# Performance work log

Measured on AMD Instinct MI355X. Metric: run time of the kernel, lower is better.

## Reference

```python
import jax, jax.numpy as jnp
import numpy as np


def _ternary(x, delta):
    # {-1, 0, +1} thresholded at +/- delta
    return jnp.where(x > delta, 1.0, jnp.where(x < -delta, -1.0, 0.0)).astype(x.dtype)


def setup_inputs() -> dict:
    key = jax.random.key(0)
    kx, kw = jax.random.split(key)
    x = jax.random.normal(kx, (8192, 4096), dtype=jnp.float32)
    weight = jax.random.normal(kw, (4096, 4096), dtype=jnp.float32) * 0.02
    return {"x": x, "weight": weight}


def reference(x, weight):
    # TernaryActivation: delta = 0.1 * mean|x|
    x_q = _ternary(x, 0.1 * jnp.mean(jnp.abs(x)))
    # TernaryQuantize: delta = 0.05 * mean|w|, scaled by alpha = mean|w|
    w_abs_mean = jnp.mean(jnp.abs(weight))
    w_q = w_abs_mean * _ternary(weight, 0.05 * w_abs_mean)
    # F.linear(x_q, w_q) = x_q @ w_q.T
    return jnp.einsum('bi,oi->bo', x_q, w_q)
```

## Files before the change

kernel.cpp:

```cpp
#include <hip/hip_runtime.h>
#include <stdint.h>

typedef __attribute__((ext_vector_type(4))) int i32x4;
typedef __attribute__((ext_vector_type(8))) int i32x8;
typedef __attribute__((ext_vector_type(4))) float f32x4;

#define MROWS 8192L
#define NCOLS 4096L
#define KDIM  4096L

#define XQ_BYTES   (MROWS * KDIM / 2)
#define WQ_BYTES   (NCOLS * KDIM / 2)
#define SCAL_OFF   (XQ_BYTES + WQ_BYTES)

__global__ __launch_bounds__(256) void k_reduce_abs(const float* __restrict__ x,
                                                    const float* __restrict__ w,
                                                    float* __restrict__ partials) {
    __shared__ float sm[256];
    int b = blockIdx.x;
    int t = threadIdx.x;
    const float4* v;
    long base;
    if (b < 512) { v = (const float4*)x; base = (long)b * 16384; }
    else         { v = (const float4*)w; base = (long)(b - 512) * 16384; }
    float s = 0.f;
    for (int i = t; i < 16384; i += 256) {
        float4 q = v[base + i];
        s += fabsf(q.x) + fabsf(q.y) + fabsf(q.z) + fabsf(q.w);
    }
    sm[t] = s;
    __syncthreads();
    for (int off = 128; off > 0; off >>= 1) {
        if (t < off) sm[t] += sm[t + off];
        __syncthreads();
    }
    if (t == 0) partials[b] = sm[0];
}

__global__ __launch_bounds__(256) void k_finalize(float* __restrict__ scal) {
    const float* partials = scal + 4;
    __shared__ double sm[256];
    int t = threadIdx.x;

    double sx = 0.0;
    for (int i = t; i < 512; i += 256) sx += (double)partials[i];
    sm[t] = sx;
    __syncthreads();
    for (int off = 128; off > 0; off >>= 1) {
        if (t < off) sm[t] += sm[t + off];
        __syncthreads();
    }
    double SX = sm[0];
    __syncthreads();

    double sw = (double)partials[512 + t];
    sm[t] = sw;
    __syncthreads();
    for (int off = 128; off > 0; off >>= 1) {
        if (t < off) sm[t] += sm[t + off];
        __syncthreads();
    }
    if (t == 0) {
        float meanx = (float)(SX / 33554432.0);
        float meanw = (float)(sm[0] / 16777216.0);
        scal[0] = 0.1f * meanx;
        scal[1] = 0.05f * meanw;
        scal[2] = meanw;
    }
}

__device__ __forceinline__ unsigned int nib4(float v, float delta) {
    return v > delta ? 2u : (v < -delta ? 10u : 0u);
}

__global__ __launch_bounds__(256) void k_quant4(const float* __restrict__ src,
                                                unsigned int* __restrict__ dst,
                                                const float* __restrict__ scal,
                                                int scal_idx, long total8) {
    float delta = scal[scal_idx];
    long i0 = (long)blockIdx.x * 256 + threadIdx.x;
    long stride = (long)gridDim.x * 256;
    const float4* s4 = (const float4*)src;
    for (long i = i0; i < total8; i += stride) {
        float4 q0 = s4[2 * i];
        float4 q1 = s4[2 * i + 1];
        unsigned int wd = nib4(q0.x, delta)
                        | (nib4(q0.y, delta) << 4)
                        | (nib4(q0.z, delta) << 8)
                        | (nib4(q0.w, delta) << 12)
                        | (nib4(q1.x, delta) << 16)
                        | (nib4(q1.y, delta) << 20)
                        | (nib4(q1.z, delta) << 24)
                        | (nib4(q1.w, delta) << 28);
        dst[i] = wd;
    }
}

#define GLOAD_LDS16(g, l)                                                             \
    __builtin_amdgcn_global_load_lds((const __attribute__((address_space(1))) void*)(g), \
                                     (__attribute__((address_space(3))) void*)(l),       \
                                     16, 0, 0)

#define MK8(v) __builtin_shufflevector((v), (v), 0, 1, 2, 3, -1, -1, -1, -1)

#define MFMA4(a, b, c)                                                        \
    __builtin_amdgcn_mfma_scale_f32_16x16x128_f8f6f4(MK8(a), MK8(b), (c),     \
        4, 4, 0, 0x7F7F7F7F, 0, 0x7F7F7F7F)

__global__ __launch_bounds__(512, 2) void k_gemm(const signed char* __restrict__ Xq,
                                                 const signed char* __restrict__ Wq,
                                                 float* __restrict__ out,
                                                 const float* __restrict__ scal) {
    __shared__ __attribute__((aligned(16))) signed char lds[131072];

    const float alpha = scal[2];

    int bid = (int)blockIdx.x;
    bid = (bid & 7) * 64 + (bid >> 3);
    int bm = bid >> 4;
    int bn = bid & 15;
    long row0 = (long)bm * 256;
    long col0 = (long)bn * 256;

    int t = threadIdx.x;
    int lane = t & 63;
    int wid = t >> 6;
    int wm = wid >> 2;
    int wn = wid & 3;

    int srow = t >> 2;
    int scol = ((t & 3) ^ ((t >> 3) & 3)) * 16;
    const signed char* Asrc = Xq + (row0 + srow) * 2048 + scol;
    const signed char* Bsrc = Wq + (col0 + srow) * 2048 + scol;
    const int ldst = wid * 1024;

#define STAGE(slot, g1) do {                                                   \
    const signed char* a_ = Asrc + (long)(g1) * 64;                            \
    const signed char* b_ = Bsrc + (long)(g1) * 64;                            \
    signed char* la_ = lds + (slot) * 32768 + ldst;                            \
    signed char* lb_ = la_ + 16384;                                            \
    GLOAD_LDS16(a_, la_);                                                      \
    GLOAD_LDS16(a_ + 128L * 2048, la_ + 8192);                                 \
    GLOAD_LDS16(b_, lb_);                                                      \
    GLOAD_LDS16(b_ + 128L * 2048, lb_ + 8192);                                 \
} while (0)

    int fr = lane & 15;
    int ck = (((lane >> 4) ^ ((fr >> 1) & 3)) << 4);
    int aoff = (wm * 128 + fr) * 64;
    int boff = 16384 + (wn * 64 + fr) * 64;

    f32x4 acc[8][4];
#pragma unroll
    for (int i = 0; i < 8; ++i)
#pragma unroll
        for (int j = 0; j < 4; ++j)
            acc[i][j] = (f32x4){0.f, 0.f, 0.f, 0.f};

    STAGE(0, 0);
    STAGE(1, 1);
    STAGE(2, 2);

    for (int g = 0; g < 32; ++g) {
        int slot = g & 3;
        __builtin_amdgcn_s_barrier();
        if (g < 29) {
            STAGE((g + 3) & 3, g + 3);
            asm volatile("s_waitcnt vmcnt(12)" ::: "memory");
        } else if (g == 29) {
            asm volatile("s_waitcnt vmcnt(8)" ::: "memory");
        } else if (g == 30) {
            asm volatile("s_waitcnt vmcnt(4)" ::: "memory");
        } else {
            asm volatile("s_waitcnt vmcnt(0)" ::: "memory");
        }
        __builtin_amdgcn_s_barrier();
        __builtin_amdgcn_sched_barrier(0);

        const signed char* A = lds + slot * 32768 + aoff;
        const signed char* B = lds + slot * 32768 + boff;

        i32x4 a0, a1, a2, a3, b0, b1, b2, b3;
        a0 = *(const i32x4*)(A + 0 * 1024 + ck);
        a1 = *(const i32x4*)(A + 1 * 1024 + ck);
        a2 = *(const i32x4*)(A + 2 * 1024 + ck);
        a3 = *(const i32x4*)(A + 3 * 1024 + ck);
        b0 = *(const i32x4*)(B + 0 * 1024 + ck);
        b1 = *(const i32x4*)(B + 1 * 1024 + ck);
        __builtin_amdgcn_s_setprio(1);
        acc[0][0] = MFMA4(a0, b0, acc[0][0]);
        acc[1][0] = MFMA4(a1, b0, acc[1][0]);
        acc[2][0] = MFMA4(a2, b0, acc[2][0]);
        acc[3][0] = MFMA4(a3, b0, acc[3][0]);
        acc[0][1] = MFMA4(a0, b1, acc[0][1]);
        acc[1][1] = MFMA4(a1, b1, acc[1][1]);
        acc[2][1] = MFMA4(a2, b1, acc[2][1]);
        acc[3][1] = MFMA4(a3, b1, acc[3][1]);
        __builtin_amdgcn_s_setprio(0);
        b2 = *(const i32x4*)(B + 2 * 1024 + ck);
        b3 = *(const i32x4*)(B + 3 * 1024 + ck);
        __builtin_amdgcn_s_setprio(1);
        acc[0][2] = MFMA4(a0, b2, acc[0][2]);
        acc[1][2] = MFMA4(a1, b2, acc[1][2]);
        acc[2][2] = MFMA4(a2, b2, acc[2][2]);
        acc[3][2] = MFMA4(a3, b2, acc[3][2]);
        acc[0][3] = MFMA4(a0, b3, acc[0][3]);
        acc[1][3] = MFMA4(a1, b3, acc[1][3]);
        acc[2][3] = MFMA4(a2, b3, acc[2][3]);
        acc[3][3] = MFMA4(a3, b3, acc[3][3]);
        __builtin_amdgcn_s_setprio(0);
        a0 = *(const i32x4*)(A + 4 * 1024 + ck);
        a1 = *(const i32x4*)(A + 5 * 1024 + ck);
        a2 = *(const i32x4*)(A + 6 * 1024 + ck);
        a3 = *(const i32x4*)(A + 7 * 1024 + ck);
        __builtin_amdgcn_s_setprio(1);
        acc[4][0] = MFMA4(a0, b0, acc[4][0]);
        acc[5][0] = MFMA4(a1, b0, acc[5][0]);
        acc[6][0] = MFMA4(a2, b0, acc[6][0]);
        acc[7][0] = MFMA4(a3, b0, acc[7][0]);
        acc[4][1] = MFMA4(a0, b1, acc[4][1]);
        acc[5][1] = MFMA4(a1, b1, acc[5][1]);
        acc[6][1] = MFMA4(a2, b1, acc[6][1]);
        acc[7][1] = MFMA4(a3, b1, acc[7][1]);
        __builtin_amdgcn_s_setprio(0);
        __builtin_amdgcn_s_setprio(1);
        acc[4][2] = MFMA4(a0, b2, acc[4][2]);
        acc[5][2] = MFMA4(a1, b2, acc[5][2]);
        acc[6][2] = MFMA4(a2, b2, acc[6][2]);
        acc[7][2] = MFMA4(a3, b2, acc[7][2]);
        acc[4][3] = MFMA4(a0, b3, acc[4][3]);
        acc[5][3] = MFMA4(a1, b3, acc[5][3]);
        acc[6][3] = MFMA4(a2, b3, acc[6][3]);
        acc[7][3] = MFMA4(a3, b3, acc[7][3]);
        __builtin_amdgcn_s_setprio(0);
    }

#pragma unroll
    for (int mi = 0; mi < 8; ++mi) {
#pragma unroll
        for (int ni = 0; ni < 4; ++ni) {
            long col = col0 + wn * 64 + ni * 16 + (lane & 15);
            long rowb = row0 + wm * 128 + mi * 16 + (lane >> 4) * 4;
#pragma unroll
            for (int r = 0; r < 4; ++r) {
                out[(rowb + r) * NCOLS + col] = alpha * acc[mi][ni][r];
            }
        }
    }
#undef STAGE
}

extern "C" void kernel_launch(void* const* d_in, const int* in_sizes, int n_in,
                              void* d_out, int out_size, void* d_ws, size_t ws_size,
                              hipStream_t stream) {
    const float* x = (const float*)d_in[0];
    const float* w = (const float*)d_in[1];
    float* out = (float*)d_out;

    uint8_t* ws = (uint8_t*)d_ws;
    signed char* Xq = (signed char*)ws;
    signed char* Wq = (signed char*)(ws + XQ_BYTES);
    float* scal = (float*)(ws + SCAL_OFF);

    k_reduce_abs<<<768, 256, 0, stream>>>(x, w, scal + 4);
    k_finalize<<<1, 256, 0, stream>>>(scal);
    k_quant4<<<2048, 256, 0, stream>>>(x, (unsigned int*)Xq, scal, 0, MROWS * KDIM / 8);
    k_quant4<<<1024, 256, 0, stream>>>(w, (unsigned int*)Wq, scal, 1, NCOLS * KDIM / 8);
    k_gemm<<<512, 512, 0, stream>>>(Xq, Wq, out, scal);
}
```

Before: 164.1 us.

## Interleave GEMM global-to-LDS prefetch with MFMA phases and merge quant kernels

The per-iteration bulk STAGE prefetch at loop top is split into four single global_load_lds issues, one inserted before each MFMA phase. Each phase is fenced with barriers and lgkmcnt waits, which shifts the vmcnt wait thresholds. This spreads memory issue across the compute phases so loads overlap with MFMA work. The two quantization launches are also merged into one kernel dispatched by block index. The extra barriers per phase add synchronization cost and could stall waves.

```diff
diff --git a/kernel.cpp b/kernel.cpp
--- a/kernel.cpp
+++ b/kernel.cpp
@@ -2,7 +2,6 @@
 #include <stdint.h>
 
 typedef __attribute__((ext_vector_type(4))) int i32x4;
-typedef __attribute__((ext_vector_type(8))) int i32x8;
 typedef __attribute__((ext_vector_type(4))) float f32x4;
 
 #define MROWS 8192L
@@ -73,13 +72,23 @@
     return v > delta ? 2u : (v < -delta ? 10u : 0u);
 }
 
-__global__ __launch_bounds__(256) void k_quant4(const float* __restrict__ src,
-                                                unsigned int* __restrict__ dst,
-                                                const float* __restrict__ scal,
-                                                int scal_idx, long total8) {
-    float delta = scal[scal_idx];
-    long i0 = (long)blockIdx.x * 256 + threadIdx.x;
-    long stride = (long)gridDim.x * 256;
+__global__ __launch_bounds__(256) void k_quant4(const float* __restrict__ x,
+                                                const float* __restrict__ w,
+                                                unsigned int* __restrict__ xq,
+                                                unsigned int* __restrict__ wq,
+                                                const float* __restrict__ scal) {
+    int b = blockIdx.x;
+    const float* src;
+    unsigned int* dst;
+    float delta;
+    long i0, stride, total8;
+    if (b < 2048) {
+        src = x; dst = xq; delta = scal[0];
+        i0 = (long)b * 256 + threadIdx.x; stride = 2048L * 256; total8 = MROWS * KDIM / 8;
+    } else {
+        src = w; dst = wq; delta = scal[1];
+        i0 = (long)(b - 2048) * 256 + threadIdx.x; stride = 1024L * 256; total8 = NCOLS * KDIM / 8;
+    }
     const float4* s4 = (const float4*)src;
     for (long i = i0; i < total8; i += stride) {
         float4 q0 = s4[2 * i];
@@ -107,6 +116,15 @@
     __builtin_amdgcn_mfma_scale_f32_16x16x128_f8f6f4(MK8(a), MK8(b), (c),     \
         4, 4, 0, 0x7F7F7F7F, 0, 0x7F7F7F7F)
 
+#define PHASE_PRE()  do {                                   \
+    __builtin_amdgcn_s_barrier();                           \
+    asm volatile("s_waitcnt lgkmcnt(0)" ::: "memory");      \
+    __builtin_amdgcn_sched_barrier(0);                      \
+    __builtin_amdgcn_s_setprio(1); } while (0)
+#define PHASE_POST() do {                                   \
+    __builtin_amdgcn_s_setprio(0);                          \
+    __builtin_amdgcn_s_barrier(); } while (0)
+
 __global__ __launch_bounds__(512, 2) void k_gemm(const signed char* __restrict__ Xq,
                                                  const signed char* __restrict__ Wq,
                                                  float* __restrict__ out,
@@ -163,11 +181,7 @@
 
     for (int g = 0; g < 32; ++g) {
         int slot = g & 3;
-        __builtin_amdgcn_s_barrier();
-        if (g < 29) {
-            STAGE((g + 3) & 3, g + 3);
-            asm volatile("s_waitcnt vmcnt(12)" ::: "memory");
-        } else if (g == 29) {
+        if (g <= 29) {
             asm volatile("s_waitcnt vmcnt(8)" ::: "memory");
         } else if (g == 30) {
             asm volatile("s_waitcnt vmcnt(4)" ::: "memory");
@@ -179,6 +193,11 @@
 
         const signed char* A = lds + slot * 32768 + aoff;
         const signed char* B = lds + slot * 32768 + boff;
+        bool st = (g <= 28);
+        const signed char* a3_ = Asrc + (long)(g + 3) * 64;
+        const signed char* b3_ = Bsrc + (long)(g + 3) * 64;
+        signed char* la3_ = lds + ((g + 3) & 3) * 32768 + ldst;
+        signed char* lb3_ = la3_ + 16384;
 
         i32x4 a0, a1, a2, a3, b0, b1, b2, b3;
         a0 = *(const i32x4*)(A + 0 * 1024 + ck);
@@ -187,7 +206,8 @@
         a3 = *(const i32x4*)(A + 3 * 1024 + ck);
         b0 = *(const i32x4*)(B + 0 * 1024 + ck);
         b1 = *(const i32x4*)(B + 1 * 1024 + ck);
-        __builtin_amdgcn_s_setprio(1);
+        if (st) GLOAD_LDS16(a3_, la3_);
+        PHASE_PRE();
         acc[0][0] = MFMA4(a0, b0, acc[0][0]);
         acc[1][0] = MFMA4(a1, b0, acc[1][0]);
         acc[2][0] = MFMA4(a2, b0, acc[2][0]);
@@ -196,10 +216,11 @@
         acc[1][1] = MFMA4(a1, b1, acc[1][1]);
         acc[2][1] = MFMA4(a2, b1, acc[2][1]);
         acc[3][1] = MFMA4(a3, b1, acc[3][1]);
-        __builtin_amdgcn_s_setprio(0);
+        PHASE_POST();
         b2 = *(const i32x4*)(B + 2 * 1024 + ck);
         b3 = *(const i32x4*)(B + 3 * 1024 + ck);
-        __builtin_amdgcn_s_setprio(1);
+        if (st) GLOAD_LDS16(a3_ + 128L * 2048, la3_ + 8192);
+        PHASE_PRE();
         acc[0][2] = MFMA4(a0, b2, acc[0][2]);
         acc[1][2] = MFMA4(a1, b2, acc[1][2]);
         acc[2][2] = MFMA4(a2, b2, acc[2][2]);
@@ -208,12 +229,13 @@
         acc[1][3] = MFMA4(a1, b3, acc[1][3]);
         acc[2][3] = MFMA4(a2, b3, acc[2][3]);
         acc[3][3] = MFMA4(a3, b3, acc[3][3]);
-        __builtin_amdgcn_s_setprio(0);
+        PHASE_POST();
         a0 = *(const i32x4*)(A + 4 * 1024 + ck);
         a1 = *(const i32x4*)(A + 5 * 1024 + ck);
         a2 = *(const i32x4*)(A + 6 * 1024 + ck);
         a3 = *(const i32x4*)(A + 7 * 1024 + ck);
-        __builtin_amdgcn_s_setprio(1);
+        if (st) GLOAD_LDS16(b3_, lb3_);
+        PHASE_PRE();
         acc[4][0] = MFMA4(a0, b0, acc[4][0]);
         acc[5][0] = MFMA4(a1, b0, acc[5][0]);
         acc[6][0] = MFMA4(a2, b0, acc[6][0]);
@@ -222,8 +244,9 @@
         acc[5][1] = MFMA4(a1, b1, acc[5][1]);
         acc[6][1] = MFMA4(a2, b1, acc[6][1]);
         acc[7][1] = MFMA4(a3, b1, acc[7][1]);
-        __builtin_amdgcn_s_setprio(0);
-        __builtin_amdgcn_s_setprio(1);
+        PHASE_POST();
+        if (st) GLOAD_LDS16(b3_ + 128L * 2048, lb3_ + 8192);
+        PHASE_PRE();
         acc[4][2] = MFMA4(a0, b2, acc[4][2]);
         acc[5][2] = MFMA4(a1, b2, acc[5][2]);
         acc[6][2] = MFMA4(a2, b2, acc[6][2]);
@@ -264,7 +287,6 @@
 
     k_reduce_abs<<<768, 256, 0, stream>>>(x, w, scal + 4);
     k_finalize<<<1, 256, 0, stream>>>(scal);
-    k_quant4<<<2048, 256, 0, stream>>>(x, (unsigned int*)Xq, scal, 0, MROWS * KDIM / 8);
-    k_quant4<<<1024, 256, 0, stream>>>(w, (unsigned int*)Wq, scal, 1, NCOLS * KDIM / 8);
+    k_quant4<<<3072, 256, 0, stream>>>(x, w, (unsigned int*)Xq, (unsigned int*)Wq, scal);
     k_gemm<<<512, 512, 0, stream>>>(Xq, Wq, out, scal);
 }
```

Measured after the change: 161.7 us. No clear change (-1.5%).

## Switch GEMM to 32x32x64 FP4 MFMA with matching LDS layout; merge quant launches

Applied to the files above, without the earlier changes.

Replaces the 16x16x128 scaled FP4 MFMA with the 32x32x64 variant. The global-to-LDS staging is re-laid out so each lane reads its 16-byte operand fragment contiguously, and the epilogue is adjusted to the 32x32 output layout. The intent is fewer MFMA and LDS-read instructions per tile and higher matrix throughput, at the cost of a new LDS layout that may introduce bank conflicts. The two quantization launches are also merged into one kernel to save a launch.

```diff
diff --git a/kernel.cpp b/kernel.cpp
--- a/kernel.cpp
+++ b/kernel.cpp
@@ -2,8 +2,7 @@
 #include <stdint.h>
 
 typedef __attribute__((ext_vector_type(4))) int i32x4;
-typedef __attribute__((ext_vector_type(8))) int i32x8;
-typedef __attribute__((ext_vector_type(4))) float f32x4;
+typedef __attribute__((ext_vector_type(16))) float f32x16;
 
 #define MROWS 8192L
 #define NCOLS 4096L
@@ -73,13 +72,23 @@
     return v > delta ? 2u : (v < -delta ? 10u : 0u);
 }
 
-__global__ __launch_bounds__(256) void k_quant4(const float* __restrict__ src,
-                                                unsigned int* __restrict__ dst,
-                                                const float* __restrict__ scal,
-                                                int scal_idx, long total8) {
-    float delta = scal[scal_idx];
-    long i0 = (long)blockIdx.x * 256 + threadIdx.x;
-    long stride = (long)gridDim.x * 256;
+__global__ __launch_bounds__(256) void k_quant4(const float* __restrict__ x,
+                                                const float* __restrict__ w,
+                                                unsigned int* __restrict__ xq,
+                                                unsigned int* __restrict__ wq,
+                                                const float* __restrict__ scal) {
+    int b = blockIdx.x;
+    const float* src;
+    unsigned int* dst;
+    float delta;
+    long i0, stride, total8;
+    if (b < 2048) {
+        src = x; dst = xq; delta = scal[0];
+        i0 = (long)b * 256 + threadIdx.x; stride = 2048L * 256; total8 = MROWS * KDIM / 8;
+    } else {
+        src = w; dst = wq; delta = scal[1];
+        i0 = (long)(b - 2048) * 256 + threadIdx.x; stride = 1024L * 256; total8 = NCOLS * KDIM / 8;
+    }
     const float4* s4 = (const float4*)src;
     for (long i = i0; i < total8; i += stride) {
         float4 q0 = s4[2 * i];
@@ -103,8 +112,8 @@
 
 #define MK8(v) __builtin_shufflevector((v), (v), 0, 1, 2, 3, -1, -1, -1, -1)
 
-#define MFMA4(a, b, c)                                                        \
-    __builtin_amdgcn_mfma_scale_f32_16x16x128_f8f6f4(MK8(a), MK8(b), (c),     \
+#define MFMA32(a, b, c)                                                       \
+    __builtin_amdgcn_mfma_scale_f32_32x32x64_f8f6f4(MK8(a), MK8(b), (c),      \
         4, 4, 0, 0x7F7F7F7F, 0, 0x7F7F7F7F)
 
 __global__ __launch_bounds__(512, 2) void k_gemm(const signed char* __restrict__ Xq,
@@ -128,34 +137,38 @@
     int wm = wid >> 2;
     int wn = wid & 3;
 
-    int srow = t >> 2;
-    int scol = ((t & 3) ^ ((t >> 3) & 3)) * 16;
-    const signed char* Asrc = Xq + (row0 + srow) * 2048 + scol;
-    const signed char* Bsrc = Wq + (col0 + srow) * 2048 + scol;
-    const int ldst = wid * 1024;
+    const signed char* sp[4];
+    int ldoff[4];
+#pragma unroll
+    for (int j = 0; j < 4; ++j) {
+        int g = wid * 4 + j;
+        ldoff[j] = g * 1024;
+        if (g < 16) {
+            long grow = row0 + (g >> 3) * 128 + ((g >> 1) & 3) * 32 + (lane & 31);
+            sp[j] = Xq + grow * 2048 + (g & 1) * 32 + (lane >> 5) * 16;
+        } else {
+            int h = g - 16;
+            long grow = col0 + (h >> 2) * 64 + ((h >> 1) & 1) * 32 + (lane & 31);
+            sp[j] = Wq + grow * 2048 + (h & 1) * 32 + (lane >> 5) * 16;
+        }
+    }
 
 #define STAGE(slot, g1) do {                                                   \
-    const signed char* a_ = Asrc + (long)(g1) * 64;                            \
-    const signed char* b_ = Bsrc + (long)(g1) * 64;                            \
-    signed char* la_ = lds + (slot) * 32768 + ldst;                            \
-    signed char* lb_ = la_ + 16384;                                            \
-    GLOAD_LDS16(a_, la_);                                                      \
-    GLOAD_LDS16(a_ + 128L * 2048, la_ + 8192);                                 \
-    GLOAD_LDS16(b_, lb_);                                                      \
-    GLOAD_LDS16(b_ + 128L * 2048, lb_ + 8192);                                 \
+    signed char* sb_ = lds + (slot) * 32768;                                   \
+    _Pragma("unroll")                                                          \
+    for (int j_ = 0; j_ < 4; ++j_)                                             \
+        GLOAD_LDS16(sp[j_] + (long)(g1) * 64, sb_ + ldoff[j_]);                \
 } while (0)
 
-    int fr = lane & 15;
-    int ck = (((lane >> 4) ^ ((fr >> 1) & 3)) << 4);
-    int aoff = (wm * 128 + fr) * 64;
-    int boff = 16384 + (wn * 64 + fr) * 64;
-
-    f32x4 acc[8][4];
-#pragma unroll
-    for (int i = 0; i < 8; ++i)
-#pragma unroll
-        for (int j = 0; j < 4; ++j)
-            acc[i][j] = (f32x4){0.f, 0.f, 0.f, 0.f};
+    const signed char* Ab = lds + wm * 8192 + lane * 16;
+    const signed char* Bb = lds + 16384 + wn * 4096 + lane * 16;
+
+    f32x16 acc[4][2];
+#pragma unroll
+    for (int i = 0; i < 4; ++i)
+#pragma unroll
+        for (int j = 0; j < 2; ++j)
+            acc[i][j] = (f32x16){0.f};
 
     STAGE(0, 0);
     STAGE(1, 1);
@@ -177,73 +190,55 @@
         __builtin_amdgcn_s_barrier();
         __builtin_amdgcn_sched_barrier(0);
 
-        const signed char* A = lds + slot * 32768 + aoff;
-        const signed char* B = lds + slot * 32768 + boff;
-
-        i32x4 a0, a1, a2, a3, b0, b1, b2, b3;
-        a0 = *(const i32x4*)(A + 0 * 1024 + ck);
-        a1 = *(const i32x4*)(A + 1 * 1024 + ck);
-        a2 = *(const i32x4*)(A + 2 * 1024 + ck);
-        a3 = *(const i32x4*)(A + 3 * 1024 + ck);
-        b0 = *(const i32x4*)(B + 0 * 1024 + ck);
-        b1 = *(const i32x4*)(B + 1 * 1024 + ck);
+        const signed char* A = Ab + slot * 32768;
+        const signed char* B = Bb + slot * 32768;
+
+        i32x4 a00, a01, a10, a11, a20, a21, a30, a31;
+        i32x4 b00, b01, b10, b11;
+        b00 = *(const i32x4*)(B + 0 * 1024);
+        b01 = *(const i32x4*)(B + 1 * 1024);
+        b10 = *(const i32x4*)(B + 2 * 1024);
+        b11 = *(const i32x4*)(B + 3 * 1024);
+        a00 = *(const i32x4*)(A + 0 * 1024);
+        a01 = *(const i32x4*)(A + 1 * 1024);
+        a10 = *(const i32x4*)(A + 2 * 1024);
+        a11 = *(const i32x4*)(A + 3 * 1024);
         __builtin_amdgcn_s_setprio(1);
-        acc[0][0] = MFMA4(a0, b0, acc[0][0]);
-        acc[1][0] = MFMA4(a1, b0, acc[1][0]);
-        acc[2][0] = MFMA4(a2, b0, acc[2][0]);
-        acc[3][0] = MFMA4(a3, b0, acc[3][0]);
-        acc[0][1] = MFMA4(a0, b1, acc[0][1]);
-        acc[1][1] = MFMA4(a1, b1, acc[1][1]);
-        acc[2][1] = MFMA4(a2, b1, acc[2][1]);
-        acc[3][1] = MFMA4(a3, b1, acc[3][1]);
+        acc[0][0] = MFMA32(a00, b00, acc[0][0]);
+        acc[0][1] = MFMA32(a00, b10, acc[0][1]);
+        acc[1][0] = MFMA32(a10, b00, acc[1][0]);
+        acc[1][1] = MFMA32(a10, b10, acc[1][1]);
+        acc[0][0] = MFMA32(a01, b01, acc[0][0]);
+        acc[0][1] = MFMA32(a01, b11, acc[0][1]);
+        acc[1][0] = MFMA32(a11, b01, acc[1][0]);
+        acc[1][1] = MFMA32(a11, b11, acc[1][1]);
         __builtin_amdgcn_s_setprio(0);
-        b2 = *(const i32x4*)(B + 2 * 1024 + ck);
-        b3 = *(const i32x4*)(B + 3 * 1024 + ck);
+        a20 = *(const i32x4*)(A + 4 * 1024);
+        a21 = *(const i32x4*)(A + 5 * 1024);
+        a30 = *(const i32x4*)(A + 6 * 1024);
+        a31 = *(const i32x4*)(A + 7 * 1024);
         __builtin_amdgcn_s_setprio(1);
-        acc[0][2] = MFMA4(a0, b2, acc[0][2]);
-        acc[1][2] = MFMA4(a1, b2, acc[1][2]);
-        acc[2][2] = MFMA4(a2, b2, acc[2][2]);
-        acc[3][2] = MFMA4(a3, b2, acc[3][2]);
-        acc[0][3] = MFMA4(a0, b3, acc[0][3]);
-        acc[1][3] = MFMA4(a1, b3, acc[1][3]);
-        acc[2][3] = MFMA4(a2, b3, acc[2][3]);
-        acc[3][3] = MFMA4(a3, b3, acc[3][3]);
+        acc[2][0] = MFMA32(a20, b00, acc[2][0]);
+        acc[2][1] = MFMA32(a20, b10, acc[2][1]);
+        acc[3][0] = MFMA32(a30, b00, acc[3][0]);
+        acc[3][1] = MFMA32(a30, b10, acc[3][1]);
+        acc[2][0] = MFMA32(a21, b01, acc[2][0]);
+        acc[2][1] = MFMA32(a21, b11, acc[2][1]);
+        acc[3][0] = MFMA32(a31, b01, acc[3][0]);
+        acc[3][1] = MFMA32(a31, b11, acc[3][1]);
         __builtin_amdgcn_s_setprio(0);
-        a0 = *(const i32x4*)(A + 4 * 1024 + ck);
-        a1 = *(const i32x4*)(A + 5 * 1024 + ck);
-        a2 = *(const i32x4*)(A + 6 * 1024 + ck);
-        a3 = *(const i32x4*)(A + 7 * 1024 + ck);
-        __builtin_amdgcn_s_setprio(1);
-        acc[4][0] = MFMA4(a0, b0, acc[4][0]);
-        acc[5][0] = MFMA4(a1, b0, acc[5][0]);
-        acc[6][0] = MFMA4(a2, b0, acc[6][0]);
-        acc[7][0] = MFMA4(a3, b0, acc[7][0]);
-        acc[4][1] = MFMA4(a0, b1, acc[4][1]);
-        acc[5][1] = MFMA4(a1, b1, acc[5][1]);
-        acc[6][1] = MFMA4(a2, b1, acc[6][1]);
-        acc[7][1] = MFMA4(a3, b1, acc[7][1]);
-        __builtin_amdgcn_s_setprio(0);
-        __builtin_amdgcn_s_setprio(1);
-        acc[4][2] = MFMA4(a0, b2, acc[4][2]);
-        acc[5][2] = MFMA4(a1, b2, acc[5][2]);
-        acc[6][2] = MFMA4(a2, b2, acc[6][2]);
-        acc[7][2] = MFMA4(a3, b2, acc[7][2]);
-        acc[4][3] = MFMA4(a0, b3, acc[4][3]);
-        acc[5][3] = MFMA4(a1, b3, acc[5][3]);
-        acc[6][3] = MFMA4(a2, b3, acc[6][3]);
-        acc[7][3] = MFMA4(a3, b3, acc[7][3]);
-        __builtin_amdgcn_s_setprio(0);
-    }
-
-#pragma unroll
-    for (int mi = 0; mi < 8; ++mi) {
-#pragma unroll
-        for (int ni = 0; ni < 4; ++ni) {
-            long col = col0 + wn * 64 + ni * 16 + (lane & 15);
-            long rowb = row0 + wm * 128 + mi * 16 + (lane >> 4) * 4;
-#pragma unroll
-            for (int r = 0; r < 4; ++r) {
-                out[(rowb + r) * NCOLS + col] = alpha * acc[mi][ni][r];
+    }
+
+#pragma unroll
+    for (int mi = 0; mi < 4; ++mi) {
+#pragma unroll
+        for (int ni = 0; ni < 2; ++ni) {
+            long col = col0 + wn * 64 + ni * 32 + (lane & 31);
+            long rowb = row0 + wm * 128 + mi * 32 + 4 * (lane >> 5);
+#pragma unroll
+            for (int r = 0; r < 16; ++r) {
+                long row = rowb + (r & 3) + 8 * (r >> 2);
+                out[row * NCOLS + col] = alpha * acc[mi][ni][r];
             }
         }
     }
@@ -264,7 +259,6 @@
 
     k_reduce_abs<<<768, 256, 0, stream>>>(x, w, scal + 4);
     k_finalize<<<1, 256, 0, stream>>>(scal);
-    k_quant4<<<2048, 256, 0, stream>>>(x, (unsigned int*)Xq, scal, 0, MROWS * KDIM / 8);
-    k_quant4<<<1024, 256, 0, stream>>>(w, (unsigned int*)Wq, scal, 1, NCOLS * KDIM / 8);
+    k_quant4<<<3072, 256, 0, stream>>>(x, w, (unsigned int*)Xq, (unsigned int*)Wq, scal);
     k_gemm<<<512, 512, 0, stream>>>(Xq, Wq, out, scal);
 }
```

New measurement: 179.4 us. 9.3% more time.
